# Kernel tuning notes

Hardware: AMD Instinct MI355X
Metric: run time of the kernel (lower is better)

Reference implementation:

```python
import jax, jax.numpy as jnp
import numpy as np

B, L, D, H = 2, 2048, 1024, 16
DK = D // H  # 64

def setup_inputs() -> dict:
    key = jax.random.key(0)
    ks = jax.random.split(key, 9)
    s = 1.0 / np.sqrt(D)
    return {
        "X":  jax.random.normal(ks[0], (B, L, D), dtype=jnp.float32),
        "WQ": jax.random.uniform(ks[1], (D, H * DK), jnp.float32, -s, s),
        "bQ": jax.random.uniform(ks[2], (H * DK,), jnp.float32, -s, s),
        "WK": jax.random.uniform(ks[3], (D, H * DK), jnp.float32, -s, s),
        "bK": jax.random.uniform(ks[4], (H * DK,), jnp.float32, -s, s),
        "WV": jax.random.uniform(ks[5], (D, H * DK), jnp.float32, -s, s),
        "bV": jax.random.uniform(ks[6], (H * DK,), jnp.float32, -s, s),
        "WO": jax.random.uniform(ks[7], (H * DK, D), jnp.float32, -s, s),
        "bO": jax.random.uniform(ks[8], (D,), jnp.float32, -s, s),
    }

def reference(X, WQ, bQ, WK, bK, WV, bV, WO, bO):
    b, l, d = X.shape
    # Linear projections, split into heads: (b, h, l, d_k)
    Q = (X @ WQ + bQ).reshape(b, l, H, DK).transpose(0, 2, 1, 3)
    K = (X @ WK + bK).reshape(b, l, H, DK).transpose(0, 2, 1, 3)
    V = (X @ WV + bV).reshape(b, l, H, DK).transpose(0, 2, 1, 3)
    # Full L x L scores (mask=None path: all-ones mask is a no-op)
    scores = jnp.einsum('bhqd,bhkd->bhqk', Q, K) / jnp.sqrt(jnp.float32(DK))
    A = jax.nn.softmax(scores, axis=-1)
    out = jnp.einsum('bhqk,bhkd->bhqd', A, V)          # (b, h, l, d_v)
    out = out.transpose(0, 2, 1, 3).reshape(b, l, H * DK)
    return out @ WO + bO
```

## Files before the change

kernel.cpp:

```cpp
#include <hip/hip_runtime.h>
#include <stdint.h>

#define BB 2
#define HH 16
#define LL 2048
#define DD 1024

typedef __bf16 b16x8 __attribute__((ext_vector_type(8)));
typedef __bf16 b16x4 __attribute__((ext_vector_type(4)));
typedef float f32x4 __attribute__((ext_vector_type(4)));

__device__ __forceinline__ short f2bf(float f) {
  unsigned u = __builtin_bit_cast(unsigned, f);
  return (short)((u + 0x7fffu + ((u >> 16) & 1u)) >> 16);
}

__device__ __forceinline__ short bfc(float f) {
  return __builtin_bit_cast(short, static_cast<__bf16>(f));
}

__device__ __forceinline__ void gl_lds16(const void* gp, void* lp) {
  __builtin_amdgcn_global_load_lds(
      (const __attribute__((address_space(1))) void*)gp,
      (__attribute__((address_space(3))) void*)lp, 16, 0, 0);
}

__global__ __launch_bounds__(256) void xcvt(const float* __restrict__ X,
                                            short* __restrict__ Xb) {
  int i = blockIdx.x * 256 + threadIdx.x;
  float4 v = ((const float4*)X)[i];
  short4 o;
  o.x = f2bf(v.x); o.y = f2bf(v.y); o.z = f2bf(v.z); o.w = f2bf(v.w);
  ((short4*)Xb)[i] = o;
}

__global__ __launch_bounds__(256) void wtrans(const float* __restrict__ W0,
                                              const float* __restrict__ W1,
                                              const float* __restrict__ W2,
                                              const float* __restrict__ W3,
                                              short* __restrict__ Wt) {
  __shared__ float t[32][33];
  const float* W = blockIdx.z == 0 ? W0 : blockIdx.z == 1 ? W1
                 : blockIdx.z == 2 ? W2 : W3;
  short* dst = Wt + (size_t)blockIdx.z * DD * DD;
  int tx = threadIdx.x & 31, ty0 = threadIdx.x >> 5;
  int nb = blockIdx.x * 32, kb = blockIdx.y * 32;
#pragma unroll
  for (int i = 0; i < 4; ++i)
    t[ty0 + i * 8][tx] = W[(size_t)(kb + ty0 + i * 8) * DD + nb + tx];
  __syncthreads();
#pragma unroll
  for (int i = 0; i < 4; ++i)
    dst[(size_t)(nb + ty0 + i * 8) * DD + kb + tx] = f2bf(t[tx][ty0 + i * 8]);
}

__global__ __launch_bounds__(256) void qkv_gemm(const short* __restrict__ Xb,
                                                const short* __restrict__ Wall,
                                                const float* __restrict__ bQ,
                                                const float* __restrict__ bK,
                                                const float* __restrict__ bV,
                                                short* __restrict__ Qo,
                                                short* __restrict__ Ko,
                                                short* __restrict__ Vto) {
  __shared__ __align__(16) short As[128 * 32];
  __shared__ __align__(16) short Bs[128 * 32];

  const int tid = threadIdx.x;
  const int lane = tid & 63;
  const int wid = tid >> 6;
  const int m0 = blockIdx.y * 128;
  const int ng = blockIdx.x * 128;
  const int sel = ng >> 10;
  const int n0 = ng & 1023;
  const short* W = Wall + (size_t)sel * DD * DD;

  const int wrow = wid >> 1, wcol = wid & 1;
  const int lrow = lane & 15;
  const int lk8 = (lane >> 4) * 8;
  const int srow = lane >> 2;
  const int scol = (lane & 3) * 8;

  f32x4 z4 = {0.f, 0.f, 0.f, 0.f};
  f32x4 acc[4][4];
#pragma unroll
  for (int i = 0; i < 4; ++i)
#pragma unroll
    for (int j = 0; j < 4; ++j) acc[i][j] = z4;

  for (int kt = 0; kt < DD; kt += 32) {
#pragma unroll
    for (int i = 0; i < 2; ++i) {
      int c = wid * 2 + i;
      gl_lds16(Xb + (size_t)(m0 + c * 16 + srow) * DD + kt + scol, As + c * 512);
      gl_lds16(W + (size_t)(n0 + c * 16 + srow) * DD + kt + scol, Bs + c * 512);
    }
    __syncthreads();
    b16x8 a[4], b[4];
#pragma unroll
    for (int i = 0; i < 4; ++i)
      a[i] = *(const b16x8*)(As + (wrow * 64 + i * 16 + lrow) * 32 + lk8);
#pragma unroll
    for (int j = 0; j < 4; ++j)
      b[j] = *(const b16x8*)(Bs + (wcol * 64 + j * 16 + lrow) * 32 + lk8);
#pragma unroll
    for (int i = 0; i < 4; ++i)
#pragma unroll
      for (int j = 0; j < 4; ++j)
        acc[i][j] = __builtin_amdgcn_mfma_f32_16x16x32_bf16(a[i], b[j], acc[i][j], 0, 0, 0);
    __syncthreads();
  }

  const float* bias = sel == 0 ? bQ : sel == 1 ? bK : bV;
  float bv[4];
#pragma unroll
  for (int j = 0; j < 4; ++j) bv[j] = bias[n0 + wcol * 64 + j * 16 + lrow];

  const int rbase = (lane >> 4) * 4;
  if (sel == 2) {
#pragma unroll
    for (int i = 0; i < 4; ++i) {
      int gm = m0 + wrow * 64 + i * 16 + rbase;
      int bb = gm >> 11, lb = gm & 2047;
      int x = lb & 63;
      int kf = x >> 4;
      int lbp = (lb & ~63) | ((kf >> 1) << 5) | (((x >> 2) & 3) << 3) | ((kf & 1) << 2);
#pragma unroll
      for (int j = 0; j < 4; ++j) {
        int gn = n0 + wcol * 64 + j * 16 + lrow;
        int h = gn >> 6, dk = gn & 63;
        short4 pk;
        pk.x = bfc(acc[i][j][0] + bv[j]);
        pk.y = bfc(acc[i][j][1] + bv[j]);
        pk.z = bfc(acc[i][j][2] + bv[j]);
        pk.w = bfc(acc[i][j][3] + bv[j]);
        *(short4*)(Vto + ((size_t)((bb * HH + h) * 64 + dk)) * LL + lbp) = pk;
      }
    }
  } else {
    short* dst = sel == 0 ? Qo : Ko;
    float sc = sel == 0 ? 0.18033688011112042f : 1.0f;
#pragma unroll
    for (int i = 0; i < 4; ++i) {
      int gm = m0 + wrow * 64 + i * 16 + rbase;
#pragma unroll
      for (int j = 0; j < 4; ++j) {
        int gn = n0 + wcol * 64 + j * 16 + lrow;
        int h = gn >> 6, dk = gn & 63;
#pragma unroll
        for (int r = 0; r < 4; ++r) {
          int m = gm + r;
          int bb = m >> 11, lq = m & 2047;
          dst[((size_t)(bb * HH + h) * LL + lq) * 64 + dk] =
              bfc((acc[i][j][r] + bv[j]) * sc);
        }
      }
    }
  }
}

__global__ __launch_bounds__(256, 2) void attn(const short* __restrict__ Qg,
                                               const short* __restrict__ Kg,
                                               const short* __restrict__ Vt,
                                               short* __restrict__ Og) {
  __shared__ __align__(16) short Ks[3][64 * 64];
  __shared__ __align__(16) short Vs[3][64 * 64];

  const int tid = threadIdx.x;
  const int lane = tid & 63;
  const int wid = tid >> 6;

  const int orig = blockIdx.x + 16 * blockIdx.y;
  const int nid = (orig & 7) * 64 + (orig >> 3);
  const int bh = nid >> 4;
  const int q0 = (nid & 15) * 128 + wid * 32;

  const short* Qb = Qg + (size_t)bh * LL * 64;
  const short* Kb = Kg + (size_t)bh * LL * 64;
  const short* Vb = Vt + (size_t)bh * 64 * LL;

  const int lrow = lane & 15;
  const int hi = lane >> 4;
  const int hi8 = hi * 8;
  const int hi16b = hi * 16;
  const int r8 = lane >> 3;
  const int c8 = lane & 7;
  const int swz8 = (c8 ^ r8) * 8;

  b16x8 qf[2][2];
#pragma unroll
  for (int f = 0; f < 2; ++f)
#pragma unroll
    for (int ks = 0; ks < 2; ++ks)
      qf[f][ks] = *(const b16x8*)(Qb + (size_t)(q0 + f * 16 + lrow) * 64 + ks * 32 + hi8);

  f32x4 z4 = {0.f, 0.f, 0.f, 0.f};
  f32x4 accO[2][4];
  float m_i[2], l_i[2];
#pragma unroll
  for (int f = 0; f < 2; ++f) {
#pragma unroll
    for (int d = 0; d < 4; ++d) accO[f][d] = z4;
    m_i[f] = -1e30f; l_i[f] = 0.f;
  }

  auto stage = [&](int kt_, int buf_) {
#pragma unroll
    for (int i = 0; i < 2; ++i) {
      int c = wid * 2 + i;
      gl_lds16(Kb + (size_t)(kt_ * 64 + c * 8 + r8) * 64 + swz8, &Ks[buf_][c * 512]);
      gl_lds16(Vb + (size_t)(c * 8 + r8) * LL + kt_ * 64 + swz8, &Vs[buf_][c * 512]);
    }
  };

  stage(0, 0);
  stage(1, 1);
  asm volatile("s_waitcnt vmcnt(4)" ::: "memory");
  __builtin_amdgcn_s_barrier();

  int cur = 0;
  for (int kt = 0; kt < LL / 64; ++kt) {
    if (kt + 2 < LL / 64) {
      int pb = cur + 2;
      if (pb >= 3) pb -= 3;
      stage(kt + 2, pb);
    }

    const short* ksb = &Ks[cur][0];
    const short* vsb = &Vs[cur][0];

    f32x4 sacc[2][4];
#pragma unroll
    for (int f = 0; f < 2; ++f)
#pragma unroll
      for (int kf = 0; kf < 4; ++kf) sacc[f][kf] = z4;

    __builtin_amdgcn_s_setprio(1);
#pragma unroll
    for (int kf = 0; kf < 4; ++kf) {
      int key = kf * 16 + lrow;
      int sw = (key & 7) << 4;
#pragma unroll
      for (int ks = 0; ks < 2; ++ks) {
        b16x8 kfr = *(const b16x8*)(ksb + key * 64 + (((ks * 64 + hi16b) ^ sw) >> 1));
#pragma unroll
        for (int f = 0; f < 2; ++f)
          sacc[f][kf] =
              __builtin_amdgcn_mfma_f32_16x16x32_bf16(kfr, qf[f][ks], sacc[f][kf], 0, 0, 0);
      }
    }
    __builtin_amdgcn_s_setprio(0);

    float lm[2];
#pragma unroll
    for (int f = 0; f < 2; ++f) {
      float mx = sacc[f][0][0];
#pragma unroll
      for (int kf = 0; kf < 4; ++kf)
#pragma unroll
        for (int r = 0; r < 4; ++r) mx = fmaxf(mx, sacc[f][kf][r]);
      lm[f] = mx;
    }
    float w = fmaxf(lm[0] - m_i[0], lm[1] - m_i[1]);

    if (!__all(w <= 8.0f)) {
#pragma unroll
      for (int f = 0; f < 2; ++f) {
        float mx = lm[f];
        mx = fmaxf(mx, __shfl_xor(mx, 16));
        mx = fmaxf(mx, __shfl_xor(mx, 32));
        float mnew = fmaxf(m_i[f], mx);
        float corr = __builtin_amdgcn_exp2f(m_i[f] - mnew);
        l_i[f] *= corr;
        m_i[f] = mnew;
#pragma unroll
        for (int d = 0; d < 4; ++d) accO[f][d] *= corr;
      }
    }

    b16x8 pfr[2][2];
#pragma unroll
    for (int f = 0; f < 2; ++f) {
      float ps = 0.f;
#pragma unroll
      for (int kf = 0; kf < 4; ++kf)
#pragma unroll
        for (int r = 0; r < 4; ++r) {
          float p = __builtin_amdgcn_exp2f(sacc[f][kf][r] - m_i[f]);
          ps += p;
          pfr[f][kf >> 1][(kf & 1) * 4 + r] = static_cast<__bf16>(p);
        }
      l_i[f] += ps;
    }

    b16x8 vfr[4][2];
#pragma unroll
    for (int db = 0; db < 4; ++db) {
      int row = db * 16 + lrow;
      int sw = (row & 7) << 4;
#pragma unroll
      for (int ks = 0; ks < 2; ++ks)
        vfr[db][ks] = *(const b16x8*)(vsb + row * 64 + (((ks * 64 + hi16b) ^ sw) >> 1));
    }

    __builtin_amdgcn_s_setprio(1);
#pragma unroll
    for (int f = 0; f < 2; ++f)
#pragma unroll
      for (int db = 0; db < 4; ++db)
#pragma unroll
        for (int ks = 0; ks < 2; ++ks)
          accO[f][db] =
              __builtin_amdgcn_mfma_f32_16x16x32_bf16(vfr[db][ks], pfr[f][ks], accO[f][db], 0, 0, 0);
    __builtin_amdgcn_s_setprio(0);

    if (kt + 2 < LL / 64) {
      asm volatile("s_waitcnt vmcnt(4)" ::: "memory");
      __builtin_amdgcn_s_barrier();
    } else if (kt + 1 < LL / 64) {
      asm volatile("s_waitcnt vmcnt(0)" ::: "memory");
      __builtin_amdgcn_s_barrier();
    }
    cur = cur + 1 >= 3 ? 0 : cur + 1;
  }

  const int bb = bh >> 4, h = bh & 15;
#pragma unroll
  for (int f = 0; f < 2; ++f) {
    float l = l_i[f];
    l += __shfl_xor(l, 16);
    l += __shfl_xor(l, 32);
    float rl = 1.0f / l;
    int q = q0 + f * 16 + lrow;
#pragma unroll
    for (int db = 0; db < 4; ++db) {
      short4 pk;
      pk.x = bfc(accO[f][db][0] * rl);
      pk.y = bfc(accO[f][db][1] * rl);
      pk.z = bfc(accO[f][db][2] * rl);
      pk.w = bfc(accO[f][db][3] * rl);
      *(short4*)(Og + (size_t)(bb * LL + q) * DD + h * 64 + db * 16 + hi * 4) = pk;
    }
  }
}

__global__ __launch_bounds__(256) void out_gemm(const short* __restrict__ Ab,
                                                const short* __restrict__ Wt,
                                                const float* __restrict__ bO,
                                                float* __restrict__ Out) {
  __shared__ __align__(16) short As[128 * 32];
  __shared__ __align__(16) short Bs[128 * 32];

  const int tid = threadIdx.x;
  const int lane = tid & 63;
  const int wid = tid >> 6;
  const int m0 = blockIdx.y * 128;
  const int n0 = blockIdx.x * 128;

  const int wrow = wid >> 1, wcol = wid & 1;
  const int lrow = lane & 15;
  const int lk8 = (lane >> 4) * 8;
  const int srow = lane >> 2;
  const int scol = (lane & 3) * 8;

  f32x4 z4 = {0.f, 0.f, 0.f, 0.f};
  f32x4 acc[4][4];
#pragma unroll
  for (int i = 0; i < 4; ++i)
#pragma unroll
    for (int j = 0; j < 4; ++j) acc[i][j] = z4;

  for (int kt = 0; kt < DD; kt += 32) {
#pragma unroll
    for (int i = 0; i < 2; ++i) {
      int c = wid * 2 + i;
      gl_lds16(Ab + (size_t)(m0 + c * 16 + srow) * DD + kt + scol, As + c * 512);
      gl_lds16(Wt + (size_t)(n0 + c * 16 + srow) * DD + kt + scol, Bs + c * 512);
    }
    __syncthreads();
    b16x8 a[4], b[4];
#pragma unroll
    for (int i = 0; i < 4; ++i)
      a[i] = *(const b16x8*)(As + (wrow * 64 + i * 16 + lrow) * 32 + lk8);
#pragma unroll
    for (int j = 0; j < 4; ++j)
      b[j] = *(const b16x8*)(Bs + (wcol * 64 + j * 16 + lrow) * 32 + lk8);
#pragma unroll
    for (int i = 0; i < 4; ++i)
#pragma unroll
      for (int j = 0; j < 4; ++j)
        acc[i][j] = __builtin_amdgcn_mfma_f32_16x16x32_bf16(a[i], b[j], acc[i][j], 0, 0, 0);
    __syncthreads();
  }

  float bv[4];
#pragma unroll
  for (int j = 0; j < 4; ++j) bv[j] = bO[n0 + wcol * 64 + j * 16 + lrow];

  const int rbase = (lane >> 4) * 4;
#pragma unroll
  for (int i = 0; i < 4; ++i) {
    int gm = m0 + wrow * 64 + i * 16 + rbase;
#pragma unroll
    for (int j = 0; j < 4; ++j) {
      int gn = n0 + wcol * 64 + j * 16 + lrow;
#pragma unroll
      for (int r = 0; r < 4; ++r)
        Out[(size_t)(gm + r) * DD + gn] = acc[i][j][r] + bv[j];
    }
  }
}

extern "C" void kernel_launch(void* const* d_in, const int* in_sizes, int n_in,
                              void* d_out, int out_size, void* d_ws, size_t ws_size,
                              hipStream_t stream) {
  const float* X = (const float*)d_in[0];
  const float* WQ = (const float*)d_in[1];
  const float* bQ = (const float*)d_in[2];
  const float* WK = (const float*)d_in[3];
  const float* bK = (const float*)d_in[4];
  const float* WV = (const float*)d_in[5];
  const float* bV = (const float*)d_in[6];
  const float* WO = (const float*)d_in[7];
  const float* bO = (const float*)d_in[8];
  float* Out = (float*)d_out;

  if (ws_size < (size_t)24 * 1024 * 1024 * 2) return;
  short* ws = (short*)d_ws;
  short* Xb = ws;
  short* Wt = Xb + (size_t)4096 * 1024;
  short* Qb = Wt + (size_t)4 * 1024 * 1024;
  short* Kb = Qb + (size_t)4096 * 1024;
  short* Vtb = Kb + (size_t)4096 * 1024;
  short* At = Vtb + (size_t)4096 * 1024;

  hipLaunchKernelGGL(xcvt, dim3(4096), dim3(256), 0, stream, X, Xb);
  hipLaunchKernelGGL(wtrans, dim3(32, 32, 4), dim3(256), 0, stream, WQ, WK, WV, WO, Wt);
  hipLaunchKernelGGL(qkv_gemm, dim3(24, 32), dim3(256), 0, stream, Xb, Wt, bQ, bK, bV,
                     Qb, Kb, Vtb);
  hipLaunchKernelGGL(attn, dim3(16, 32), dim3(256), 0, stream, Qb, Kb, Vtb, At);
  hipLaunchKernelGGL(out_gemm, dim3(8, 32), dim3(256), 0, stream, At,
                     Wt + (size_t)3 * 1024 * 1024, bO, Out);
}
```

Measured before the change: 115.7 us.

## Software-pipeline attention over paired KV tiles, remap GEMM blocks, shrink out_gemm tiles

```diff
diff --git a/kernel.cpp b/kernel.cpp
--- a/kernel.cpp
+++ b/kernel.cpp
@@ -7,8 +7,8 @@
 #define DD 1024
 
 typedef __bf16 b16x8 __attribute__((ext_vector_type(8)));
-typedef __bf16 b16x4 __attribute__((ext_vector_type(4)));
 typedef float f32x4 __attribute__((ext_vector_type(4)));
+typedef int i32x4 __attribute__((ext_vector_type(4)));
 
 __device__ __forceinline__ short f2bf(float f) {
   unsigned u = __builtin_bit_cast(unsigned, f);
@@ -17,6 +17,12 @@
 
 __device__ __forceinline__ short bfc(float f) {
   return __builtin_bit_cast(short, static_cast<__bf16>(f));
+}
+
+__device__ __forceinline__ int cvtpk(float lo, float hi) {
+  int r;
+  asm("v_cvt_pk_bf16_f32 %0, %1, %2" : "=v"(r) : "v"(lo), "v"(hi));
+  return r;
 }
 
 __device__ __forceinline__ void gl_lds16(const void* gp, void* lp) {
@@ -68,8 +74,10 @@
   const int tid = threadIdx.x;
   const int lane = tid & 63;
   const int wid = tid >> 6;
-  const int m0 = blockIdx.y * 128;
-  const int ng = blockIdx.x * 128;
+  const int orig = blockIdx.x + 24 * blockIdx.y;
+  const int nid = (orig & 7) * 96 + (orig >> 3);
+  const int m0 = (nid & 31) * 128;
+  const int ng = (nid >> 5) * 128;
   const int sel = ng >> 10;
   const int n0 = ng & 1023;
   const short* W = Wall + (size_t)sel * DD * DD;
@@ -162,8 +170,8 @@
                                                const short* __restrict__ Kg,
                                                const short* __restrict__ Vt,
                                                short* __restrict__ Og) {
-  __shared__ __align__(16) short Ks[3][64 * 64];
-  __shared__ __align__(16) short Vs[3][64 * 64];
+  __shared__ __align__(16) short Ks[4][64 * 64];
+  __shared__ __align__(16) short Vs[4][64 * 64];
 
   const int tid = threadIdx.x;
   const int lane = tid & 63;
@@ -203,125 +211,138 @@
     m_i[f] = -1e30f; l_i[f] = 0.f;
   }
 
-  auto stage = [&](int kt_, int buf_) {
-#pragma unroll
-    for (int i = 0; i < 2; ++i) {
-      int c = wid * 2 + i;
-      gl_lds16(Kb + (size_t)(kt_ * 64 + c * 8 + r8) * 64 + swz8, &Ks[buf_][c * 512]);
-      gl_lds16(Vb + (size_t)(c * 8 + r8) * LL + kt_ * 64 + swz8, &Vs[buf_][c * 512]);
-    }
-  };
-
-  stage(0, 0);
-  stage(1, 1);
-  asm volatile("s_waitcnt vmcnt(4)" ::: "memory");
+  int offs[4][2];
+#pragma unroll
+  for (int a = 0; a < 4; ++a) {
+    int row = a * 16 + lrow;
+    int sw = (row & 7) << 4;
+#pragma unroll
+    for (int ks = 0; ks < 2; ++ks)
+      offs[a][ks] = row * 128 + ((ks * 64 + hi16b) ^ sw);
+  }
+
+#define STAGE(KT, SL)                                                         \
+  {                                                                           \
+    _Pragma("unroll") for (int i = 0; i < 2; ++i) {                           \
+      int c = wid * 2 + i;                                                    \
+      gl_lds16(Kb + (size_t)((KT) * 64 + c * 8 + r8) * 64 + swz8,             \
+               &Ks[SL][c * 512]);                                             \
+      gl_lds16(Vb + (size_t)(c * 8 + r8) * LL + (KT) * 64 + swz8,             \
+               &Vs[SL][c * 512]);                                             \
+    }                                                                         \
+  }
+
+#define QKPH(SL, SACC)                                                       \
+  {                                                                          \
+    const char* ksb = (const char*)&Ks[SL][0];                               \
+    _Pragma("unroll") for (int f = 0; f < 2; ++f)                            \
+        _Pragma("unroll") for (int kf = 0; kf < 4; ++kf) SACC[f][kf] = z4;   \
+    __builtin_amdgcn_s_setprio(1);                                           \
+    _Pragma("unroll") for (int kf = 0; kf < 4; ++kf)                         \
+        _Pragma("unroll") for (int ks = 0; ks < 2; ++ks) {                   \
+      b16x8 kfr = *(const b16x8*)(ksb + offs[kf][ks]);                       \
+      _Pragma("unroll") for (int f = 0; f < 2; ++f)                          \
+          SACC[f][kf] = __builtin_amdgcn_mfma_f32_16x16x32_bf16(             \
+              kfr, qf[f][ks], SACC[f][kf], 0, 0, 0);                         \
+    }                                                                        \
+    __builtin_amdgcn_s_setprio(0);                                           \
+  }
+
+#define SMPH(SACC, PFR)                                                      \
+  {                                                                          \
+    float lm[2];                                                             \
+    _Pragma("unroll") for (int f = 0; f < 2; ++f) {                          \
+      float mx = fmaxf(fmaxf(SACC[f][0][0], SACC[f][0][1]),                  \
+                       fmaxf(SACC[f][0][2], SACC[f][0][3]));                 \
+      _Pragma("unroll") for (int kf = 1; kf < 4; ++kf)                       \
+          mx = fmaxf(mx, fmaxf(fmaxf(SACC[f][kf][0], SACC[f][kf][1]),        \
+                               fmaxf(SACC[f][kf][2], SACC[f][kf][3])));      \
+      lm[f] = mx;                                                            \
+    }                                                                        \
+    float w = fmaxf(lm[0] - m_i[0], lm[1] - m_i[1]);                         \
+    if (!__all(w <= 8.0f)) {                                                 \
+      _Pragma("unroll") for (int f = 0; f < 2; ++f) {                        \
+        float mx = lm[f];                                                    \
+        mx = fmaxf(mx, __shfl_xor(mx, 16));                                  \
+        mx = fmaxf(mx, __shfl_xor(mx, 32));                                  \
+        float mnew = fmaxf(m_i[f], mx);                                      \
+        float corr = __builtin_amdgcn_exp2f(m_i[f] - mnew);                  \
+        l_i[f] *= corr;                                                      \
+        m_i[f] = mnew;                                                       \
+        _Pragma("unroll") for (int d = 0; d < 4; ++d) accO[f][d] *= corr;    \
+      }                                                                      \
+    }                                                                        \
+    _Pragma("unroll") for (int f = 0; f < 2; ++f) {                          \
+      float ps = 0.f;                                                        \
+      _Pragma("unroll") for (int c = 0; c < 2; ++c) {                        \
+        float e0 = __builtin_amdgcn_exp2f(SACC[f][2 * c][0] - m_i[f]);       \
+        float e1 = __builtin_amdgcn_exp2f(SACC[f][2 * c][1] - m_i[f]);       \
+        float e2 = __builtin_amdgcn_exp2f(SACC[f][2 * c][2] - m_i[f]);       \
+        float e3 = __builtin_amdgcn_exp2f(SACC[f][2 * c][3] - m_i[f]);       \
+        float e4 = __builtin_amdgcn_exp2f(SACC[f][2 * c + 1][0] - m_i[f]);   \
+        float e5 = __builtin_amdgcn_exp2f(SACC[f][2 * c + 1][1] - m_i[f]);   \
+        float e6 = __builtin_amdgcn_exp2f(SACC[f][2 * c + 1][2] - m_i[f]);   \
+        float e7 = __builtin_amdgcn_exp2f(SACC[f][2 * c + 1][3] - m_i[f]);   \
+        ps += ((e0 + e1) + (e2 + e3)) + ((e4 + e5) + (e6 + e7));             \
+        i32x4 pt;                                                            \
+        pt[0] = cvtpk(e0, e1);                                               \
+        pt[1] = cvtpk(e2, e3);                                               \
+        pt[2] = cvtpk(e4, e5);                                               \
+        pt[3] = cvtpk(e6, e7);                                               \
+        PFR[f][c] = __builtin_bit_cast(b16x8, pt);                           \
+      }                                                                      \
+      l_i[f] += ps;                                                          \
+    }                                                                        \
+  }
+
+#define PVPH(SL, PFR)                                                        \
+  {                                                                          \
+    const char* vsb = (const char*)&Vs[SL][0];                               \
+    __builtin_amdgcn_s_setprio(1);                                           \
+    _Pragma("unroll") for (int db = 0; db < 4; ++db) {                       \
+      b16x8 v0 = *(const b16x8*)(vsb + offs[db][0]);                         \
+      b16x8 v1 = *(const b16x8*)(vsb + offs[db][1]);                         \
+      _Pragma("unroll") for (int f = 0; f < 2; ++f) {                        \
+        accO[f][db] = __builtin_amdgcn_mfma_f32_16x16x32_bf16(               \
+            v0, PFR[f][0], accO[f][db], 0, 0, 0);                            \
+        accO[f][db] = __builtin_amdgcn_mfma_f32_16x16x32_bf16(               \
+            v1, PFR[f][1], accO[f][db], 0, 0, 0);                            \
+      }                                                                      \
+    }                                                                        \
+    __builtin_amdgcn_s_setprio(0);                                           \
+  }
+
+#define BODY(B0, B1, KT, PF)                                                 \
+  {                                                                          \
+    if (PF) { STAGE((KT) + 2, (B0) ^ 2); STAGE((KT) + 3, ((B0) ^ 2) + 1); }  \
+    f32x4 sA[2][4], sB[2][4];                                                \
+    b16x8 pA[2][2], pB[2][2];                                                \
+    QKPH(B0, sA);                                                            \
+    SMPH(sA, pA);                                                            \
+    QKPH(B1, sB);                                                            \
+    PVPH(B0, pA);                                                            \
+    SMPH(sB, pB);                                                            \
+    PVPH(B1, pB);                                                            \
+    if (PF) {                                                                \
+      asm volatile("s_waitcnt vmcnt(0)" ::: "memory");                       \
+      __builtin_amdgcn_s_barrier();                                          \
+    }                                                                        \
+  }
+
+  STAGE(0, 0);
+  STAGE(1, 1);
+  asm volatile("s_waitcnt vmcnt(0)" ::: "memory");
   __builtin_amdgcn_s_barrier();
 
-  int cur = 0;
-  for (int kt = 0; kt < LL / 64; ++kt) {
-    if (kt + 2 < LL / 64) {
-      int pb = cur + 2;
-      if (pb >= 3) pb -= 3;
-      stage(kt + 2, pb);
-    }
-
-    const short* ksb = &Ks[cur][0];
-    const short* vsb = &Vs[cur][0];
-
-    f32x4 sacc[2][4];
-#pragma unroll
-    for (int f = 0; f < 2; ++f)
-#pragma unroll
-      for (int kf = 0; kf < 4; ++kf) sacc[f][kf] = z4;
-
-    __builtin_amdgcn_s_setprio(1);
-#pragma unroll
-    for (int kf = 0; kf < 4; ++kf) {
-      int key = kf * 16 + lrow;
-      int sw = (key & 7) << 4;
-#pragma unroll
-      for (int ks = 0; ks < 2; ++ks) {
-        b16x8 kfr = *(const b16x8*)(ksb + key * 64 + (((ks * 64 + hi16b) ^ sw) >> 1));
-#pragma unroll
-        for (int f = 0; f < 2; ++f)
-          sacc[f][kf] =
-              __builtin_amdgcn_mfma_f32_16x16x32_bf16(kfr, qf[f][ks], sacc[f][kf], 0, 0, 0);
-      }
-    }
-    __builtin_amdgcn_s_setprio(0);
-
-    float lm[2];
-#pragma unroll
-    for (int f = 0; f < 2; ++f) {
-      float mx = sacc[f][0][0];
-#pragma unroll
-      for (int kf = 0; kf < 4; ++kf)
-#pragma unroll
-        for (int r = 0; r < 4; ++r) mx = fmaxf(mx, sacc[f][kf][r]);
-      lm[f] = mx;
-    }
-    float w = fmaxf(lm[0] - m_i[0], lm[1] - m_i[1]);
-
-    if (!__all(w <= 8.0f)) {
-#pragma unroll
-      for (int f = 0; f < 2; ++f) {
-        float mx = lm[f];
-        mx = fmaxf(mx, __shfl_xor(mx, 16));
-        mx = fmaxf(mx, __shfl_xor(mx, 32));
-        float mnew = fmaxf(m_i[f], mx);
-        float corr = __builtin_amdgcn_exp2f(m_i[f] - mnew);
-        l_i[f] *= corr;
-        m_i[f] = mnew;
-#pragma unroll
-        for (int d = 0; d < 4; ++d) accO[f][d] *= corr;
-      }
-    }
-
-    b16x8 pfr[2][2];
-#pragma unroll
-    for (int f = 0; f < 2; ++f) {
-      float ps = 0.f;
-#pragma unroll
-      for (int kf = 0; kf < 4; ++kf)
-#pragma unroll
-        for (int r = 0; r < 4; ++r) {
-          float p = __builtin_amdgcn_exp2f(sacc[f][kf][r] - m_i[f]);
-          ps += p;
-          pfr[f][kf >> 1][(kf & 1) * 4 + r] = static_cast<__bf16>(p);
-        }
-      l_i[f] += ps;
-    }
-
-    b16x8 vfr[4][2];
-#pragma unroll
-    for (int db = 0; db < 4; ++db) {
-      int row = db * 16 + lrow;
-      int sw = (row & 7) << 4;
-#pragma unroll
-      for (int ks = 0; ks < 2; ++ks)
-        vfr[db][ks] = *(const b16x8*)(vsb + row * 64 + (((ks * 64 + hi16b) ^ sw) >> 1));
-    }
-
-    __builtin_amdgcn_s_setprio(1);
-#pragma unroll
-    for (int f = 0; f < 2; ++f)
-#pragma unroll
-      for (int db = 0; db < 4; ++db)
-#pragma unroll
-        for (int ks = 0; ks < 2; ++ks)
-          accO[f][db] =
-              __builtin_amdgcn_mfma_f32_16x16x32_bf16(vfr[db][ks], pfr[f][ks], accO[f][db], 0, 0, 0);
-    __builtin_amdgcn_s_setprio(0);
-
-    if (kt + 2 < LL / 64) {
-      asm volatile("s_waitcnt vmcnt(4)" ::: "memory");
-      __builtin_amdgcn_s_barrier();
-    } else if (kt + 1 < LL / 64) {
-      asm volatile("s_waitcnt vmcnt(0)" ::: "memory");
-      __builtin_amdgcn_s_barrier();
-    }
-    cur = cur + 1 >= 3 ? 0 : cur + 1;
-  }
+  for (int it = 0; it < 8; ++it) {
+    BODY(0, 1, it * 4, 1);
+    BODY(2, 3, it * 4 + 2, it < 7);
+  }
+#undef BODY
+#undef PVPH
+#undef SMPH
+#undef QKPH
+#undef STAGE
 
   const int bb = bh >> 4, h = bh & 15;
 #pragma unroll
@@ -347,14 +368,16 @@
                                                 const short* __restrict__ Wt,
                                                 const float* __restrict__ bO,
                                                 float* __restrict__ Out) {
-  __shared__ __align__(16) short As[128 * 32];
+  __shared__ __align__(16) short As[64 * 32];
   __shared__ __align__(16) short Bs[128 * 32];
 
   const int tid = threadIdx.x;
   const int lane = tid & 63;
   const int wid = tid >> 6;
-  const int m0 = blockIdx.y * 128;
-  const int n0 = blockIdx.x * 128;
+  const int orig = blockIdx.x + 8 * blockIdx.y;
+  const int nid = (orig & 7) * 64 + (orig >> 3);
+  const int n0 = (nid >> 6) * 128;
+  const int m0 = (nid & 63) * 64;
 
   const int wrow = wid >> 1, wcol = wid & 1;
   const int lrow = lane & 15;
@@ -363,29 +386,29 @@
   const int scol = (lane & 3) * 8;
 
   f32x4 z4 = {0.f, 0.f, 0.f, 0.f};
-  f32x4 acc[4][4];
-#pragma unroll
-  for (int i = 0; i < 4; ++i)
+  f32x4 acc[2][4];
+#pragma unroll
+  for (int i = 0; i < 2; ++i)
 #pragma unroll
     for (int j = 0; j < 4; ++j) acc[i][j] = z4;
 
   for (int kt = 0; kt < DD; kt += 32) {
+    gl_lds16(Ab + (size_t)(m0 + wid * 16 + srow) * DD + kt + scol, As + wid * 512);
 #pragma unroll
     for (int i = 0; i < 2; ++i) {
       int c = wid * 2 + i;
-      gl_lds16(Ab + (size_t)(m0 + c * 16 + srow) * DD + kt + scol, As + c * 512);
       gl_lds16(Wt + (size_t)(n0 + c * 16 + srow) * DD + kt + scol, Bs + c * 512);
     }
     __syncthreads();
-    b16x8 a[4], b[4];
-#pragma unroll
-    for (int i = 0; i < 4; ++i)
-      a[i] = *(const b16x8*)(As + (wrow * 64 + i * 16 + lrow) * 32 + lk8);
+    b16x8 a[2], b[4];
+#pragma unroll
+    for (int i = 0; i < 2; ++i)
+      a[i] = *(const b16x8*)(As + (wrow * 32 + i * 16 + lrow) * 32 + lk8);
 #pragma unroll
     for (int j = 0; j < 4; ++j)
       b[j] = *(const b16x8*)(Bs + (wcol * 64 + j * 16 + lrow) * 32 + lk8);
 #pragma unroll
-    for (int i = 0; i < 4; ++i)
+    for (int i = 0; i < 2; ++i)
 #pragma unroll
       for (int j = 0; j < 4; ++j)
         acc[i][j] = __builtin_amdgcn_mfma_f32_16x16x32_bf16(a[i], b[j], acc[i][j], 0, 0, 0);
@@ -398,8 +421,8 @@
 
   const int rbase = (lane >> 4) * 4;
 #pragma unroll
-  for (int i = 0; i < 4; ++i) {
-    int gm = m0 + wrow * 64 + i * 16 + rbase;
+  for (int i = 0; i < 2; ++i) {
+    int gm = m0 + wrow * 32 + i * 16 + rbase;
 #pragma unroll
     for (int j = 0; j < 4; ++j) {
       int gn = n0 + wcol * 64 + j * 16 + lrow;
@@ -438,6 +461,6 @@
   hipLaunchKernelGGL(qkv_gemm, dim3(24, 32), dim3(256), 0, stream, Xb, Wt, bQ, bK, bV,
                      Qb, Kb, Vtb);
   hipLaunchKernelGGL(attn, dim3(16, 32), dim3(256), 0, stream, Qb, Kb, Vtb, At);
-  hipLaunchKernelGGL(out_gemm, dim3(8, 32), dim3(256), 0, stream, At,
+  hipLaunchKernelGGL(out_gemm, dim3(8, 64), dim3(256), 0, stream, At,
                      Wt + (size_t)3 * 1024 * 1024, bO, Out);
 }
```

Measured after the change: 111.8 us. 3.3% less time.

## Remap GEMM block order for XCDs, shrink out-GEMM tile, tidy attention inner loop

Applied to the files above, without the earlier changes.

```diff
diff --git a/kernel.cpp b/kernel.cpp
--- a/kernel.cpp
+++ b/kernel.cpp
@@ -7,8 +7,8 @@
 #define DD 1024
 
 typedef __bf16 b16x8 __attribute__((ext_vector_type(8)));
-typedef __bf16 b16x4 __attribute__((ext_vector_type(4)));
 typedef float f32x4 __attribute__((ext_vector_type(4)));
+typedef int i32x4 __attribute__((ext_vector_type(4)));
 
 __device__ __forceinline__ short f2bf(float f) {
   unsigned u = __builtin_bit_cast(unsigned, f);
@@ -17,6 +17,12 @@
 
 __device__ __forceinline__ short bfc(float f) {
   return __builtin_bit_cast(short, static_cast<__bf16>(f));
+}
+
+__device__ __forceinline__ int cvtpk(float lo, float hi) {
+  int r;
+  asm("v_cvt_pk_bf16_f32 %0, %1, %2" : "=v"(r) : "v"(lo), "v"(hi));
+  return r;
 }
 
 __device__ __forceinline__ void gl_lds16(const void* gp, void* lp) {
@@ -68,8 +74,10 @@
   const int tid = threadIdx.x;
   const int lane = tid & 63;
   const int wid = tid >> 6;
-  const int m0 = blockIdx.y * 128;
-  const int ng = blockIdx.x * 128;
+  const int orig = blockIdx.x + 24 * blockIdx.y;
+  const int nid = (orig & 7) * 96 + (orig >> 3);
+  const int m0 = (nid & 31) * 128;
+  const int ng = (nid >> 5) * 128;
   const int sel = ng >> 10;
   const int n0 = ng & 1023;
   const short* W = Wall + (size_t)sel * DD * DD;
@@ -203,6 +211,16 @@
     m_i[f] = -1e30f; l_i[f] = 0.f;
   }
 
+  int offs[4][2];
+#pragma unroll
+  for (int a = 0; a < 4; ++a) {
+    int row = a * 16 + lrow;
+    int sw = (row & 7) << 4;
+#pragma unroll
+    for (int ks = 0; ks < 2; ++ks)
+      offs[a][ks] = row * 128 + ((ks * 64 + hi16b) ^ sw);
+  }
+
   auto stage = [&](int kt_, int buf_) {
 #pragma unroll
     for (int i = 0; i < 2; ++i) {
@@ -225,8 +243,8 @@
       stage(kt + 2, pb);
     }
 
-    const short* ksb = &Ks[cur][0];
-    const short* vsb = &Vs[cur][0];
+    const char* ksb = (const char*)&Ks[cur][0];
+    const char* vsb = (const char*)&Vs[cur][0];
 
     f32x4 sacc[2][4];
 #pragma unroll
@@ -237,11 +255,9 @@
     __builtin_amdgcn_s_setprio(1);
 #pragma unroll
     for (int kf = 0; kf < 4; ++kf) {
-      int key = kf * 16 + lrow;
-      int sw = (key & 7) << 4;
 #pragma unroll
       for (int ks = 0; ks < 2; ++ks) {
-        b16x8 kfr = *(const b16x8*)(ksb + key * 64 + (((ks * 64 + hi16b) ^ sw) >> 1));
+        b16x8 kfr = *(const b16x8*)(ksb + offs[kf][ks]);
 #pragma unroll
         for (int f = 0; f < 2; ++f)
           sacc[f][kf] =
@@ -253,11 +269,12 @@
     float lm[2];
 #pragma unroll
     for (int f = 0; f < 2; ++f) {
-      float mx = sacc[f][0][0];
-#pragma unroll
-      for (int kf = 0; kf < 4; ++kf)
-#pragma unroll
-        for (int r = 0; r < 4; ++r) mx = fmaxf(mx, sacc[f][kf][r]);
+      float mx = fmaxf(fmaxf(sacc[f][0][0], sacc[f][0][1]),
+                       fmaxf(sacc[f][0][2], sacc[f][0][3]));
+#pragma unroll
+      for (int kf = 1; kf < 4; ++kf)
+        mx = fmaxf(mx, fmaxf(fmaxf(sacc[f][kf][0], sacc[f][kf][1]),
+                             fmaxf(sacc[f][kf][2], sacc[f][kf][3])));
       lm[f] = mx;
     }
     float w = fmaxf(lm[0] - m_i[0], lm[1] - m_i[1]);
@@ -282,35 +299,45 @@
     for (int f = 0; f < 2; ++f) {
       float ps = 0.f;
 #pragma unroll
-      for (int kf = 0; kf < 4; ++kf)
-#pragma unroll
-        for (int r = 0; r < 4; ++r) {
-          float p = __builtin_amdgcn_exp2f(sacc[f][kf][r] - m_i[f]);
-          ps += p;
-          pfr[f][kf >> 1][(kf & 1) * 4 + r] = static_cast<__bf16>(p);
-        }
+      for (int c = 0; c < 2; ++c) {
+        float e0 = __builtin_amdgcn_exp2f(sacc[f][2 * c][0] - m_i[f]);
+        float e1 = __builtin_amdgcn_exp2f(sacc[f][2 * c][1] - m_i[f]);
+        float e2 = __builtin_amdgcn_exp2f(sacc[f][2 * c][2] - m_i[f]);
+        float e3 = __builtin_amdgcn_exp2f(sacc[f][2 * c][3] - m_i[f]);
+        float e4 = __builtin_amdgcn_exp2f(sacc[f][2 * c + 1][0] - m_i[f]);
+        float e5 = __builtin_amdgcn_exp2f(sacc[f][2 * c + 1][1] - m_i[f]);
+        float e6 = __builtin_amdgcn_exp2f(sacc[f][2 * c + 1][2] - m_i[f]);
+        float e7 = __builtin_amdgcn_exp2f(sacc[f][2 * c + 1][3] - m_i[f]);
+        ps += ((e0 + e1) + (e2 + e3)) + ((e4 + e5) + (e6 + e7));
+        i32x4 pt;
+        pt[0] = cvtpk(e0, e1);
+        pt[1] = cvtpk(e2, e3);
+        pt[2] = cvtpk(e4, e5);
+        pt[3] = cvtpk(e6, e7);
+        pfr[f][c] = __builtin_bit_cast(b16x8, pt);
+      }
       l_i[f] += ps;
     }
 
     b16x8 vfr[4][2];
 #pragma unroll
     for (int db = 0; db < 4; ++db) {
-      int row = db * 16 + lrow;
-      int sw = (row & 7) << 4;
 #pragma unroll
       for (int ks = 0; ks < 2; ++ks)
-        vfr[db][ks] = *(const b16x8*)(vsb + row * 64 + (((ks * 64 + hi16b) ^ sw) >> 1));
+        vfr[db][ks] = *(const b16x8*)(vsb + offs[db][ks]);
     }
 
     __builtin_amdgcn_s_setprio(1);
 #pragma unroll
-    for (int f = 0; f < 2; ++f)
-#pragma unroll
-      for (int db = 0; db < 4; ++db)
-#pragma unroll
-        for (int ks = 0; ks < 2; ++ks)
-          accO[f][db] =
-              __builtin_amdgcn_mfma_f32_16x16x32_bf16(vfr[db][ks], pfr[f][ks], accO[f][db], 0, 0, 0);
+    for (int f = 0; f < 2; ++f) {
+#pragma unroll
+      for (int db = 0; db < 4; ++db) {
+        accO[f][db] = __builtin_amdgcn_mfma_f32_16x16x32_bf16(vfr[db][0], pfr[f][0],
+                                                              accO[f][db], 0, 0, 0);
+        accO[f][db] = __builtin_amdgcn_mfma_f32_16x16x32_bf16(vfr[db][1], pfr[f][1],
+                                                              accO[f][db], 0, 0, 0);
+      }
+    }
     __builtin_amdgcn_s_setprio(0);
 
     if (kt + 2 < LL / 64) {
@@ -347,14 +374,16 @@
                                                 const short* __restrict__ Wt,
                                                 const float* __restrict__ bO,
                                                 float* __restrict__ Out) {
-  __shared__ __align__(16) short As[128 * 32];
+  __shared__ __align__(16) short As[64 * 32];
   __shared__ __align__(16) short Bs[128 * 32];
 
   const int tid = threadIdx.x;
   const int lane = tid & 63;
   const int wid = tid >> 6;
-  const int m0 = blockIdx.y * 128;
-  const int n0 = blockIdx.x * 128;
+  const int orig = blockIdx.x + 8 * blockIdx.y;
+  const int nid = (orig & 7) * 64 + (orig >> 3);
+  const int n0 = (nid >> 6) * 128;
+  const int m0 = (nid & 63) * 64;
 
   const int wrow = wid >> 1, wcol = wid & 1;
   const int lrow = lane & 15;
@@ -363,29 +392,29 @@
   const int scol = (lane & 3) * 8;
 
   f32x4 z4 = {0.f, 0.f, 0.f, 0.f};
-  f32x4 acc[4][4];
-#pragma unroll
-  for (int i = 0; i < 4; ++i)
+  f32x4 acc[2][4];
+#pragma unroll
+  for (int i = 0; i < 2; ++i)
 #pragma unroll
     for (int j = 0; j < 4; ++j) acc[i][j] = z4;
 
   for (int kt = 0; kt < DD; kt += 32) {
+    gl_lds16(Ab + (size_t)(m0 + wid * 16 + srow) * DD + kt + scol, As + wid * 512);
 #pragma unroll
     for (int i = 0; i < 2; ++i) {
       int c = wid * 2 + i;
-      gl_lds16(Ab + (size_t)(m0 + c * 16 + srow) * DD + kt + scol, As + c * 512);
       gl_lds16(Wt + (size_t)(n0 + c * 16 + srow) * DD + kt + scol, Bs + c * 512);
     }
     __syncthreads();
-    b16x8 a[4], b[4];
-#pragma unroll
-    for (int i = 0; i < 4; ++i)
-      a[i] = *(const b16x8*)(As + (wrow * 64 + i * 16 + lrow) * 32 + lk8);
+    b16x8 a[2], b[4];
+#pragma unroll
+    for (int i = 0; i < 2; ++i)
+      a[i] = *(const b16x8*)(As + (wrow * 32 + i * 16 + lrow) * 32 + lk8);
 #pragma unroll
     for (int j = 0; j < 4; ++j)
       b[j] = *(const b16x8*)(Bs + (wcol * 64 + j * 16 + lrow) * 32 + lk8);
 #pragma unroll
-    for (int i = 0; i < 4; ++i)
+    for (int i = 0; i < 2; ++i)
 #pragma unroll
       for (int j = 0; j < 4; ++j)
         acc[i][j] = __builtin_amdgcn_mfma_f32_16x16x32_bf16(a[i], b[j], acc[i][j], 0, 0, 0);
@@ -398,8 +427,8 @@
 
   const int rbase = (lane >> 4) * 4;
 #pragma unroll
-  for (int i = 0; i < 4; ++i) {
-    int gm = m0 + wrow * 64 + i * 16 + rbase;
+  for (int i = 0; i < 2; ++i) {
+    int gm = m0 + wrow * 32 + i * 16 + rbase;
 #pragma unroll
     for (int j = 0; j < 4; ++j) {
       int gn = n0 + wcol * 64 + j * 16 + lrow;
@@ -438,6 +467,6 @@
   hipLaunchKernelGGL(qkv_gemm, dim3(24, 32), dim3(256), 0, stream, Xb, Wt, bQ, bK, bV,
                      Qb, Kb, Vtb);
   hipLaunchKernelGGL(attn, dim3(16, 32), dim3(256), 0, stream, Qb, Kb, Vtb, At);
-  hipLaunchKernelGGL(out_gemm, dim3(8, 32), dim3(256), 0, stream, At,
+  hipLaunchKernelGGL(out_gemm, dim3(8, 64), dim3(256), 0, stream, At,
                      Wt + (size_t)3 * 1024 * 1024, bO, Out);
 }
```

Result: faster. 111.5 us (-3.6%).
